# Kernel tuning notes

Hardware: AMD Instinct MI355X
Metric: run time of the kernel (lower is better)

Reference implementation:

```python
import jax, jax.numpy as jnp
import numpy as np

N = 50000          # nodes in homogeneous graph
E_RAND = 450000    # non-self edges
R = 5              # 4 relations + identity
C = 2              # num_channels
L = 2              # num_layers
IN_DIM = 256
HID = 128
NUM_CLASS = 16
N_CAT = 10000


def setup_inputs() -> dict:
    key = jax.random.key(0)
    ks = jax.random.split(key, 10)
    h = jax.random.normal(ks[0], (N, IN_DIM), dtype=jnp.float32)
    src_r = jax.random.randint(ks[1], (E_RAND,), 0, N, dtype=jnp.int32)
    dst_r = jax.random.randint(ks[2], (E_RAND,), 0, N, dtype=jnp.int32)
    et_r = jax.random.randint(ks[3], (E_RAND,), 0, R - 1, dtype=jnp.int32)
    self_idx = jnp.arange(N, dtype=jnp.int32)
    src = jnp.concatenate([src_r, self_idx])
    dst = jnp.concatenate([dst_r, self_idx])
    etype = jnp.concatenate([et_r, jnp.full((N,), R - 1, dtype=jnp.int32)])
    category_idx = jax.random.randint(ks[4], (N_CAT,), 0, N, dtype=jnp.int32)
    # learned params
    gt_w = 0.01 * jax.random.normal(ks[5], (L, C, R), dtype=jnp.float32)
    Wc = jax.random.normal(ks[6], (C, IN_DIM, HID), dtype=jnp.float32) / np.sqrt(IN_DIM)
    W1 = jax.random.normal(ks[7], (C * HID, HID), dtype=jnp.float32) / np.sqrt(C * HID)
    b1 = jnp.zeros((HID,), dtype=jnp.float32)
    W2 = jax.random.normal(ks[8], (HID, NUM_CLASS), dtype=jnp.float32) / np.sqrt(HID)
    b2 = jnp.zeros((NUM_CLASS,), dtype=jnp.float32)
    return {"h": h, "src": src, "dst": dst, "etype": etype,
            "category_idx": category_idx, "gt_w": gt_w, "Wc": Wc,
            "W1": W1, "b1": b1, "W2": W2, "b2": b2}


def reference(h, src, dst, etype, category_idx, gt_w, Wc, W1, b1, W2, b2):
    n = h.shape[0]
    # per-channel input projection: H[c] = h @ Wc[c]  -> [C, N, HID]
    H = jnp.einsum('nd,cdh->cnh', h, Wc)
    seg = lambda v: jax.ops.segment_sum(v, dst, num_segments=n)
    for l in range(gt_w.shape[0]):
        # GTConv: per-channel softmax over relations; summed weighted adjacency
        Filt = jax.nn.softmax(gt_w[l], axis=1)        # [C, R]
        w = Filt[:, etype]                            # [C, E] edge weights
        # EdgeWeightNorm('right'): divide by weighted in-degree of dst
        deg = jax.vmap(seg)(w)                        # [C, N]
        wn = w / deg[:, dst]                          # [C, E]
        # GCNConv: sum_{e: dst=v} H[src(e)] * wn(e)
        msg = H[:, src, :] * wn[:, :, None]           # [C, E, HID]
        H = jax.vmap(seg)(msg)                        # [C, N, HID]
    # concat channels along feature dim (torch.cat(H, dim=1))
    X = jnp.transpose(H, (1, 0, 2)).reshape(n, -1)    # [N, C*HID]
    X = jax.nn.relu(X @ W1 + b1)
    y = X @ W2 + b2
    return y[category_idx]
```

## Files before the change

### kernel.cpp

```cpp
#include <hip/hip_runtime.h>
#include <hip/hip_bf16.h>

#define IN_DIM 256
#define HID 128
#define CCH 2
#define RR 5
#define LL 2
#define NCLS 16

typedef __attribute__((ext_vector_type(8))) short short8;
typedef __attribute__((ext_vector_type(4))) short short4_;
typedef __attribute__((ext_vector_type(4))) float floatx4;

__device__ __forceinline__ unsigned short f2bf(float f) {
    unsigned int u = __float_as_uint(f);
    unsigned int r = (u + 0x7FFFu + ((u >> 16) & 1u)) >> 16;
    return (unsigned short)r;
}

__global__ void cvt_weights(const float* __restrict__ Wc, const float* __restrict__ W1,
                            const float* __restrict__ gt_w,
                            unsigned short* __restrict__ WcT, unsigned short* __restrict__ W1T,
                            float* __restrict__ filt) {
    int i = blockIdx.x * 256 + threadIdx.x;
    if (blockIdx.x == 0 && threadIdx.x < LL * CCH) {
        const float* g = gt_w + threadIdx.x * RR;
        float m = -1e30f;
        for (int r = 0; r < RR; ++r) m = fmaxf(m, g[r]);
        float e[RR], s = 0.f;
        for (int r = 0; r < RR; ++r) { e[r] = __expf(g[r] - m); s += e[r]; }
        for (int r = 0; r < RR; ++r) filt[threadIdx.x * RR + r] = e[r] / s;
    }
    if (i < CCH * HID * IN_DIM) {
        int c = i >> 15;
        int rem = i & 32767;
        int d = rem >> 8;
        int k = rem & 255;
        WcT[i] = f2bf(Wc[((size_t)c * IN_DIM + k) * HID + d]);
    }
    if (i < HID * IN_DIM) {
        int d = i >> 8;
        int k = i & 255;
        W1T[i] = f2bf(W1[(size_t)k * HID + d]);
    }
}

__global__ __launch_bounds__(256, 2) void proj_mfma(const float* __restrict__ h,
                                                    const unsigned short* __restrict__ WcT,
                                                    unsigned short* __restrict__ H0, int N) {
    __shared__ unsigned short Bl[64 * 256];
    int t = threadIdx.x;
    int wv = t >> 6, l = t & 63;
    int l15 = l & 15, lq = l >> 4;
    int n0 = blockIdx.x * 64;

#pragma unroll
    for (int i = 0; i < 16; ++i) {
        int fi = t * 4 + i * 1024;
        int r = fi >> 8;
        int k = fi & 255;
        int node = n0 + r;
        const float* src = h + (size_t)(node < N ? node : N - 1) * IN_DIM + k;
        floatx4 f = *(const floatx4*)src;
        short4_ s4;
        s4[0] = (short)f2bf(f[0]); s4[1] = (short)f2bf(f[1]);
        s4[2] = (short)f2bf(f[2]); s4[3] = (short)f2bf(f[3]);
        int c = k >> 3;
        int half = (k >> 2) & 1;
        int cs = c ^ ((r & 7) << 2);
        *(short4_*)(&Bl[r * 256 + cs * 8 + half * 4]) = s4;
    }
    __syncthreads();

    floatx4 acc[4][4];
#pragma unroll
    for (int m = 0; m < 4; ++m)
#pragma unroll
        for (int n = 0; n < 4; ++n) acc[m][n] = (floatx4){0.f, 0.f, 0.f, 0.f};

#pragma unroll
    for (int kh = 0; kh < 2; ++kh) {
        short8 a[4][4];
#pragma unroll
        for (int mt0 = 0; mt0 < 4; ++mt0) {
            const unsigned short* arow = WcT + (size_t)((wv * 4 + mt0) * 16 + l15) * IN_DIM;
#pragma unroll
            for (int kk = 0; kk < 4; ++kk)
                a[mt0][kk] = *(const short8*)(arow + (kh * 4 + kk) * 32 + lq * 8);
        }
#pragma unroll
        for (int nf = 0; nf < 4; ++nf) {
            int r = nf * 16 + l15;
            short8 b[4];
#pragma unroll
            for (int kk = 0; kk < 4; ++kk) {
                int c = (kh * 4 + kk) * 4 + lq;
                int cs = c ^ ((r & 7) << 2);
                b[kk] = *(const short8*)(&Bl[r * 256 + cs * 8]);
            }
#pragma unroll
            for (int mt0 = 0; mt0 < 4; ++mt0)
#pragma unroll
                for (int kk = 0; kk < 4; ++kk)
                    acc[mt0][nf] = __builtin_amdgcn_mfma_f32_16x16x32_bf16(a[mt0][kk], b[kk],
                                                                           acc[mt0][nf], 0, 0, 0);
        }
    }

#pragma unroll
    for (int mt0 = 0; mt0 < 4; ++mt0) {
        int m0 = (wv * 4 + mt0) * 16 + lq * 4;
#pragma unroll
        for (int nf = 0; nf < 4; ++nf) {
            int node = n0 + nf * 16 + l15;
            if (node < N) {
                short4_ st;
                st[0] = (short)f2bf(acc[mt0][nf][0]); st[1] = (short)f2bf(acc[mt0][nf][1]);
                st[2] = (short)f2bf(acc[mt0][nf][2]); st[3] = (short)f2bf(acc[mt0][nf][3]);
                *(short4_*)(H0 + (size_t)node * (CCH * HID) + m0) = st;
            }
        }
    }
}

__global__ void count_kernel(const int* __restrict__ dst, int* __restrict__ counts, int E) {
    for (int e = blockIdx.x * blockDim.x + threadIdx.x; e < E; e += gridDim.x * blockDim.x)
        atomicAdd(&counts[dst[e]], 1);
}

__global__ void scanA_kernel(const int* __restrict__ counts, int* __restrict__ partials, int n) {
    __shared__ int s[256];
    int t = threadIdx.x;
    int i = blockIdx.x * 256 + t;
    int v = (i < n) ? counts[i] : 0;
    s[t] = v;
    __syncthreads();
    for (int off = 1; off < 256; off <<= 1) {
        int tv = (t >= off) ? s[t - off] : 0;
        __syncthreads();
        s[t] += tv;
        __syncthreads();
    }
    if (t == 255) partials[blockIdx.x] = s[255];
}

__global__ void scanB_kernel(const int* __restrict__ partials, int* __restrict__ chunk_off, int nchunk) {
    __shared__ int s[256];
    int t = threadIdx.x;
    int v = (t < nchunk) ? partials[t] : 0;
    s[t] = v;
    __syncthreads();
    for (int off = 1; off < 256; off <<= 1) {
        int tv = (t >= off) ? s[t - off] : 0;
        __syncthreads();
        s[t] += tv;
        __syncthreads();
    }
    if (t < nchunk) chunk_off[t] = s[t] - v;
}

__global__ void scanC_kernel(const int* __restrict__ counts, const int* __restrict__ chunk_off,
                             int* __restrict__ offsets, int* __restrict__ cursor, int n) {
    __shared__ int s[256];
    int t = threadIdx.x;
    int i = blockIdx.x * 256 + t;
    int v = (i < n) ? counts[i] : 0;
    s[t] = v;
    __syncthreads();
    for (int off = 1; off < 256; off <<= 1) {
        int tv = (t >= off) ? s[t - off] : 0;
        __syncthreads();
        s[t] += tv;
        __syncthreads();
    }
    if (i < n) {
        int incl = chunk_off[blockIdx.x] + s[t];
        offsets[i + 1] = incl;
        cursor[i] = incl - v;
    }
    if (i == 0) offsets[0] = 0;
}

__global__ void fill_kernel(const int* __restrict__ src, const int* __restrict__ dst,
                            const int* __restrict__ etype, int* __restrict__ cursor,
                            int2* __restrict__ epack, int E) {
    for (int e = blockIdx.x * blockDim.x + threadIdx.x; e < E; e += gridDim.x * blockDim.x) {
        int d = dst[e];
        int p = atomicAdd(&cursor[d], 1);
        epack[p] = make_int2(src[e], etype[e]);
    }
}

__global__ __launch_bounds__(256) void agg_kernel(const uint4* __restrict__ Hin,
                                                  uint4* __restrict__ Hout,
                                                  const int* __restrict__ offs,
                                                  const int2* __restrict__ epack,
                                                  const float* __restrict__ filt, int N) {
    int t = threadIdx.x;
    int g = t >> 5;
    int lane32 = t & 31;
    int node = blockIdx.x * 8 + g;
    if (node >= N) return;
    int c = lane32 >> 4;
    float f0 = filt[c * RR + 0], f1 = filt[c * RR + 1], f2 = filt[c * RR + 2];
    float f3 = filt[c * RR + 3], f4 = filt[c * RR + 4];

    int e0 = offs[node], e1 = offs[node + 1];
    float acc[8];
#pragma unroll
    for (int r = 0; r < 8; ++r) acc[r] = 0.f;
    float deg = 0.f;

    int2 pc = epack[e0];
    uint4 v = Hin[(size_t)pc.x * 32 + lane32];
    int et = pc.y;
    for (int j = e0 + 1; ; ++j) {
        uint4 vc = v;
        int etc = et;
        bool more = j < e1;
        if (more) {
            int2 pn = epack[j];
            v = Hin[(size_t)pn.x * 32 + lane32];
            et = pn.y;
        }
        float w = (etc == 0) ? f0 : (etc == 1) ? f1 : (etc == 2) ? f2 : (etc == 3) ? f3 : f4;
        deg += w;
        acc[0] += w * __uint_as_float(vc.x << 16);
        acc[1] += w * __uint_as_float(vc.x & 0xFFFF0000u);
        acc[2] += w * __uint_as_float(vc.y << 16);
        acc[3] += w * __uint_as_float(vc.y & 0xFFFF0000u);
        acc[4] += w * __uint_as_float(vc.z << 16);
        acc[5] += w * __uint_as_float(vc.z & 0xFFFF0000u);
        acc[6] += w * __uint_as_float(vc.w << 16);
        acc[7] += w * __uint_as_float(vc.w & 0xFFFF0000u);
        if (!more) break;
    }

    float inv = 1.f / deg;
    uint4 o;
    o.x = (unsigned int)f2bf(acc[0] * inv) | ((unsigned int)f2bf(acc[1] * inv) << 16);
    o.y = (unsigned int)f2bf(acc[2] * inv) | ((unsigned int)f2bf(acc[3] * inv) << 16);
    o.z = (unsigned int)f2bf(acc[4] * inv) | ((unsigned int)f2bf(acc[5] * inv) << 16);
    o.w = (unsigned int)f2bf(acc[6] * inv) | ((unsigned int)f2bf(acc[7] * inv) << 16);
    Hout[(size_t)node * 32 + lane32] = o;
}

__global__ __launch_bounds__(256) void mlp1_mfma(const unsigned short* __restrict__ H2,
                                                 const int* __restrict__ cat,
                                                 const unsigned short* __restrict__ W1T,
                                                 const float* __restrict__ b1,
                                                 float* __restrict__ hidden, int NCAT) {
    int t = threadIdx.x;
    int wv = t >> 6, l = t & 63;
    int l15 = l & 15, lq = l >> 4;
    int i = blockIdx.x * 64 + wv * 16 + l15;
    int iclamp = i < NCAT ? i : NCAT - 1;
    int node = cat[iclamp];

    short8 bfrag[8];
    const unsigned short* xrow = H2 + (size_t)node * (CCH * HID);
#pragma unroll
    for (int kk = 0; kk < 8; ++kk)
        bfrag[kk] = *(const short8*)(xrow + kk * 32 + lq * 8);

#pragma unroll
    for (int mt = 0; mt < 8; ++mt) {
        floatx4 acc = {0.f, 0.f, 0.f, 0.f};
        const unsigned short* arow = W1T + (size_t)(mt * 16 + l15) * (CCH * HID);
#pragma unroll
        for (int kk = 0; kk < 8; ++kk) {
            short8 a = *(const short8*)(arow + kk * 32 + lq * 8);
            acc = __builtin_amdgcn_mfma_f32_16x16x32_bf16(a, bfrag[kk], acc, 0, 0, 0);
        }
        if (i < NCAT) {
            int d0 = mt * 16 + lq * 4;
            floatx4 o;
#pragma unroll
            for (int r = 0; r < 4; ++r) o[r] = fmaxf(acc[r] + b1[d0 + r], 0.f);
            *(floatx4*)(hidden + (size_t)i * HID + d0) = o;
        }
    }
}

__global__ void mlp2_kernel(const float* __restrict__ hidden, const float* __restrict__ W2,
                            const float* __restrict__ b2, float* __restrict__ out, int NCAT) {
    int idx = blockIdx.x * 256 + threadIdx.x;
    int i = idx >> 4, cls = idx & 15;
    if (i >= NCAT) return;
    const float* hrow = hidden + (size_t)i * HID;
    float acc = b2[cls];
#pragma unroll 8
    for (int j = 0; j < HID; ++j) acc += hrow[j] * W2[j * NCLS + cls];
    out[idx] = acc;
}

extern "C" void kernel_launch(void* const* d_in, const int* in_sizes, int n_in,
                              void* d_out, int out_size, void* d_ws, size_t ws_size,
                              hipStream_t stream) {
    const float* h    = (const float*)d_in[0];
    const int* src    = (const int*)d_in[1];
    const int* dst    = (const int*)d_in[2];
    const int* etype  = (const int*)d_in[3];
    const int* cat    = (const int*)d_in[4];
    const float* gt_w = (const float*)d_in[5];
    const float* Wc   = (const float*)d_in[6];
    const float* W1   = (const float*)d_in[7];
    const float* b1   = (const float*)d_in[8];
    const float* W2   = (const float*)d_in[9];
    const float* b2   = (const float*)d_in[10];
    float* out = (float*)d_out;

    const int N = in_sizes[0] / IN_DIM;
    const int E = in_sizes[1];
    const int NCAT = in_sizes[4];
    const int NCHUNK = (N + 255) / 256;

    char* p = (char*)d_ws;
    auto alloc = [&](size_t bytes) {
        char* q = p;
        p += (bytes + 255) & ~(size_t)255;
        return q;
    };
    unsigned short* HA   = (unsigned short*)alloc((size_t)N * CCH * HID * 2);
    unsigned short* HB   = (unsigned short*)alloc((size_t)N * CCH * HID * 2);
    unsigned short* WcT  = (unsigned short*)alloc((size_t)CCH * HID * IN_DIM * 2);
    unsigned short* W1T  = (unsigned short*)alloc((size_t)HID * CCH * HID * 2);
    float* hidden        = (float*)alloc((size_t)NCAT * HID * 4);
    int*   counts        = (int*)alloc((size_t)N * 4);
    int*   offsets       = (int*)alloc((size_t)(N + 1) * 4);
    int*   cursor        = (int*)alloc((size_t)N * 4);
    int*   partials      = (int*)alloc((size_t)NCHUNK * 4);
    int*   chunk_off     = (int*)alloc((size_t)NCHUNK * 4);
    int2*  epack         = (int2*)alloc((size_t)E * 8);
    float* filt          = (float*)alloc((size_t)LL * CCH * RR * 4);

    hipMemsetAsync(counts, 0, (size_t)N * 4, stream);

    cvt_weights<<<(CCH * HID * IN_DIM + 255) / 256, 256, 0, stream>>>(Wc, W1, gt_w, WcT, W1T, filt);
    proj_mfma<<<(N + 63) / 64, 256, 0, stream>>>(h, WcT, HA, N);

    count_kernel<<<512, 256, 0, stream>>>(dst, counts, E);
    scanA_kernel<<<NCHUNK, 256, 0, stream>>>(counts, partials, N);
    scanB_kernel<<<1, 256, 0, stream>>>(partials, chunk_off, NCHUNK);
    scanC_kernel<<<NCHUNK, 256, 0, stream>>>(counts, chunk_off, offsets, cursor, N);
    fill_kernel<<<512, 256, 0, stream>>>(src, dst, etype, cursor, epack, E);

    agg_kernel<<<(N + 7) / 8, 256, 0, stream>>>((const uint4*)HA, (uint4*)HB,
                                                offsets, epack, filt, N);
    agg_kernel<<<(N + 7) / 8, 256, 0, stream>>>((const uint4*)HB, (uint4*)HA,
                                                offsets, epack, filt + CCH * RR, N);

    mlp1_mfma<<<(NCAT + 63) / 64, 256, 0, stream>>>(HA, cat, W1T, b1, hidden, NCAT);
    mlp2_kernel<<<(NCAT * NCLS + 255) / 256, 256, 0, stream>>>(hidden, W2, b2, out, NCAT);
}
```

Before: 296.7 us.

## Prefetch edge lists via shuffles, double-buffer gathers, fuse MLP layers

The aggregation kernel now loads up to 32 edge records per node in one coalesced read and hands them out with warp shuffles. It keeps two feature gathers in flight (distance-2 prefetch) instead of one, which targets the serialized pointer-chasing latency of the per-edge loop. Separately, the two MLP kernels are fused so the hidden activations stay in shared memory, removing one launch and a global round trip. The cost is more registers in the aggregation loop and an extra global-load path for nodes with more than 32 edges.

Result: faster. 290.6 us (-2.1%).

```diff
diff --git a/kernel.cpp b/kernel.cpp
--- a/kernel.cpp
+++ b/kernel.cpp
@@ -191,6 +191,23 @@
     }
 }
 
+#define GETSRC(dn, s_, e_) do {                                     \
+    s_ = __shfl(ep.x, (dn) & 31, 32);                               \
+    e_ = __shfl(ep.y, (dn) & 31, 32);                               \
+    if ((dn) >= 32) { int2 _p = epack[e0 + (dn)]; s_ = _p.x; e_ = _p.y; } \
+} while (0)
+
+#define ACCUM(vv, ww) do {                                          \
+    acc[0] += (ww) * __uint_as_float((vv).x << 16);                 \
+    acc[1] += (ww) * __uint_as_float((vv).x & 0xFFFF0000u);         \
+    acc[2] += (ww) * __uint_as_float((vv).y << 16);                 \
+    acc[3] += (ww) * __uint_as_float((vv).y & 0xFFFF0000u);         \
+    acc[4] += (ww) * __uint_as_float((vv).z << 16);                 \
+    acc[5] += (ww) * __uint_as_float((vv).z & 0xFFFF0000u);         \
+    acc[6] += (ww) * __uint_as_float((vv).w << 16);                 \
+    acc[7] += (ww) * __uint_as_float((vv).w & 0xFFFF0000u);         \
+} while (0)
+
 __global__ __launch_bounds__(256) void agg_kernel(const uint4* __restrict__ Hin,
                                                   uint4* __restrict__ Hout,
                                                   const int* __restrict__ offs,
@@ -206,37 +223,41 @@
     float f3 = filt[c * RR + 3], f4 = filt[c * RR + 4];
 
     int e0 = offs[node], e1 = offs[node + 1];
+    int deg = e1 - e0;
+    int2 ep = epack[e0 + (lane32 < deg ? lane32 : deg - 1)];
+
     float acc[8];
 #pragma unroll
     for (int r = 0; r < 8; ++r) acc[r] = 0.f;
-    float deg = 0.f;
-
-    int2 pc = epack[e0];
-    uint4 v = Hin[(size_t)pc.x * 32 + lane32];
-    int et = pc.y;
-    for (int j = e0 + 1; ; ++j) {
-        uint4 vc = v;
-        int etc = et;
-        bool more = j < e1;
-        if (more) {
-            int2 pn = epack[j];
-            v = Hin[(size_t)pn.x * 32 + lane32];
-            et = pn.y;
-        }
-        float w = (etc == 0) ? f0 : (etc == 1) ? f1 : (etc == 2) ? f2 : (etc == 3) ? f3 : f4;
-        deg += w;
-        acc[0] += w * __uint_as_float(vc.x << 16);
-        acc[1] += w * __uint_as_float(vc.x & 0xFFFF0000u);
-        acc[2] += w * __uint_as_float(vc.y << 16);
-        acc[3] += w * __uint_as_float(vc.y & 0xFFFF0000u);
-        acc[4] += w * __uint_as_float(vc.z << 16);
-        acc[5] += w * __uint_as_float(vc.z & 0xFFFF0000u);
-        acc[6] += w * __uint_as_float(vc.w << 16);
-        acc[7] += w * __uint_as_float(vc.w & 0xFFFF0000u);
-        if (!more) break;
-    }
-
-    float inv = 1.f / deg;
+    float dw = 0.f;
+
+    uint4 va, vb;
+    int eta = 0, etb = 0;
+    { int s; GETSRC(0, s, eta); va = Hin[(size_t)s * 32 + lane32]; }
+    if (deg > 1) { int s; GETSRC(1, s, etb); vb = Hin[(size_t)s * 32 + lane32]; }
+    else vb = va;
+
+    int d = 0;
+    for (;;) {
+        {
+            float w = (eta == 0) ? f0 : (eta == 1) ? f1 : (eta == 2) ? f2 : (eta == 3) ? f3 : f4;
+            dw += w;
+            ACCUM(va, w);
+        }
+        int dn = d + 2;
+        if (dn < deg) { int s; GETSRC(dn, s, eta); va = Hin[(size_t)s * 32 + lane32]; }
+        ++d; if (d >= deg) break;
+        {
+            float w = (etb == 0) ? f0 : (etb == 1) ? f1 : (etb == 2) ? f2 : (etb == 3) ? f3 : f4;
+            dw += w;
+            ACCUM(vb, w);
+        }
+        dn = d + 2;
+        if (dn < deg) { int s; GETSRC(dn, s, etb); vb = Hin[(size_t)s * 32 + lane32]; }
+        ++d; if (d >= deg) break;
+    }
+
+    float inv = 1.f / dw;
     uint4 o;
     o.x = (unsigned int)f2bf(acc[0] * inv) | ((unsigned int)f2bf(acc[1] * inv) << 16);
     o.y = (unsigned int)f2bf(acc[2] * inv) | ((unsigned int)f2bf(acc[3] * inv) << 16);
@@ -245,11 +266,14 @@
     Hout[(size_t)node * 32 + lane32] = o;
 }
 
-__global__ __launch_bounds__(256) void mlp1_mfma(const unsigned short* __restrict__ H2,
+__global__ __launch_bounds__(256) void mlp_fused(const unsigned short* __restrict__ H2,
                                                  const int* __restrict__ cat,
                                                  const unsigned short* __restrict__ W1T,
                                                  const float* __restrict__ b1,
-                                                 float* __restrict__ hidden, int NCAT) {
+                                                 const float* __restrict__ W2,
+                                                 const float* __restrict__ b2,
+                                                 float* __restrict__ out, int NCAT) {
+    __shared__ float hidd[64][132];
     int t = threadIdx.x;
     int wv = t >> 6, l = t & 63;
     int l15 = l & 15, lq = l >> 4;
@@ -263,6 +287,7 @@
     for (int kk = 0; kk < 8; ++kk)
         bfrag[kk] = *(const short8*)(xrow + kk * 32 + lq * 8);
 
+    int nb = wv * 16 + l15;
 #pragma unroll
     for (int mt = 0; mt < 8; ++mt) {
         floatx4 acc = {0.f, 0.f, 0.f, 0.f};
@@ -272,26 +297,31 @@
             short8 a = *(const short8*)(arow + kk * 32 + lq * 8);
             acc = __builtin_amdgcn_mfma_f32_16x16x32_bf16(a, bfrag[kk], acc, 0, 0, 0);
         }
-        if (i < NCAT) {
-            int d0 = mt * 16 + lq * 4;
-            floatx4 o;
-#pragma unroll
-            for (int r = 0; r < 4; ++r) o[r] = fmaxf(acc[r] + b1[d0 + r], 0.f);
-            *(floatx4*)(hidden + (size_t)i * HID + d0) = o;
-        }
-    }
-}
-
-__global__ void mlp2_kernel(const float* __restrict__ hidden, const float* __restrict__ W2,
-                            const float* __restrict__ b2, float* __restrict__ out, int NCAT) {
-    int idx = blockIdx.x * 256 + threadIdx.x;
-    int i = idx >> 4, cls = idx & 15;
-    if (i >= NCAT) return;
-    const float* hrow = hidden + (size_t)i * HID;
-    float acc = b2[cls];
+        int d0 = mt * 16 + lq * 4;
+#pragma unroll
+        for (int r = 0; r < 4; ++r)
+            hidd[nb][d0 + r] = fmaxf(acc[r] + b1[d0 + r], 0.f);
+    }
+    __syncthreads();
+
+    int il = t >> 2;
+    int cls0 = (t & 3) * 4;
+    int i_out = blockIdx.x * 64 + il;
+    if (i_out < NCAT) {
+        float o0 = b2[cls0], o1 = b2[cls0 + 1], o2 = b2[cls0 + 2], o3 = b2[cls0 + 3];
+        const float* hr = hidd[il];
 #pragma unroll 8
-    for (int j = 0; j < HID; ++j) acc += hrow[j] * W2[j * NCLS + cls];
-    out[idx] = acc;
+        for (int j = 0; j < HID; ++j) {
+            float hv = hr[j];
+            const float* w2r = W2 + j * NCLS + cls0;
+            o0 += hv * w2r[0];
+            o1 += hv * w2r[1];
+            o2 += hv * w2r[2];
+            o3 += hv * w2r[3];
+        }
+        floatx4 o = {o0, o1, o2, o3};
+        *(floatx4*)(out + (size_t)i_out * NCLS + cls0) = o;
+    }
 }
 
 extern "C" void kernel_launch(void* const* d_in, const int* in_sizes, int n_in,
@@ -325,7 +355,6 @@
     unsigned short* HB   = (unsigned short*)alloc((size_t)N * CCH * HID * 2);
     unsigned short* WcT  = (unsigned short*)alloc((size_t)CCH * HID * IN_DIM * 2);
     unsigned short* W1T  = (unsigned short*)alloc((size_t)HID * CCH * HID * 2);
-    float* hidden        = (float*)alloc((size_t)NCAT * HID * 4);
     int*   counts        = (int*)alloc((size_t)N * 4);
     int*   offsets       = (int*)alloc((size_t)(N + 1) * 4);
     int*   cursor        = (int*)alloc((size_t)N * 4);
@@ -350,6 +379,5 @@
     agg_kernel<<<(N + 7) / 8, 256, 0, stream>>>((const uint4*)HB, (uint4*)HA,
                                                 offsets, epack, filt + CCH * RR, N);
 
-    mlp1_mfma<<<(NCAT + 63) / 64, 256, 0, stream>>>(HA, cat, W1T, b1, hidden, NCAT);
-    mlp2_kernel<<<(NCAT * NCLS + 255) / 256, 256, 0, stream>>>(hidden, W2, b2, out, NCAT);
-}
+    mlp_fused<<<(NCAT + 63) / 64, 256, 0, stream>>>(HA, cat, W1T, b1, W2, b2, out, NCAT);
+}
```
